# Kernel tuning notes

Measured on AMD Instinct MI355X. Metric: run time of the kernel, lower is better.

## Reference

```python
import jax, jax.numpy as jnp
import numpy as np

B, S, D, H, P = 2, 2048, 1024, 16, 2048  # batch, q_len, d_model, heads, past_len
DEPTH = D // H
W_STD = 0.02


def setup_inputs() -> dict:
    key = jax.random.key(0)
    ks = jax.random.split(key, 5)
    x = jax.random.normal(ks[0], (B, S, D), dtype=jnp.float32)
    past_layer = jax.random.normal(ks[1], (B, 2, H, P, DEPTH), dtype=jnp.float32)
    w_attn = jax.random.normal(ks[2], (D, 3 * D), dtype=jnp.float32) * W_STD
    b_attn = jnp.zeros((3 * D,), dtype=jnp.float32)
    w_proj = jax.random.normal(ks[3], (D, D), dtype=jnp.float32) * W_STD
    b_proj = jnp.zeros((D,), dtype=jnp.float32)
    # causal mask with KV cache: query i sits at absolute position P+i; key j
    # is masked (1.0 -> +(-1e9)) when j > P + i.
    q_pos = P + jnp.arange(S)[:, None]        # [S,1]
    k_pos = jnp.arange(P + S)[None, :]        # [1,P+S]
    mask = (k_pos > q_pos).astype(jnp.float32)[None, None]  # [1,1,S,P+S]
    return {"x": x, "mask": mask, "past_layer": past_layer,
            "w_attn": w_attn, "b_attn": b_attn,
            "w_proj": w_proj, "b_proj": b_proj}


def _split_heads(t):
    # [B,S,D] -> [B,H,S,depth]
    b, s, _ = t.shape
    return t.reshape(b, s, H, DEPTH).transpose(0, 2, 1, 3)


def reference(x, mask, past_layer, w_attn, b_attn, w_proj, b_proj):
    # fused QKV projection (Conv1d == pointwise Linear)
    qkv = jnp.einsum('bsd,de->bse', x, w_attn) + b_attn        # [B,S,3D]
    q, k, v = jnp.split(qkv, 3, axis=2)
    q, k, v = _split_heads(q), _split_heads(k), _split_heads(v)
    # KV-cache concat
    k = jnp.concatenate([past_layer[:, 0], k], axis=2)         # [B,H,P+S,depth]
    v = jnp.concatenate([past_layer[:, 1], v], axis=2)
    present = jnp.stack([k, v], axis=1)                        # [B,2,H,P+S,depth]
    # scaled dot-product attention (full score matrix, eval mode: no dropout)
    scores = jnp.einsum('bhqd,bhkd->bhqk', q, k) / jnp.sqrt(
        jnp.asarray(DEPTH, dtype=jnp.float32))
    scores = scores + mask * (-1e9)
    attn = jax.nn.softmax(scores, axis=-1)
    ctx = jnp.einsum('bhqk,bhkd->bhqd', attn, v)               # [B,H,S,depth]
    merged = ctx.transpose(0, 2, 1, 3).reshape(B, S, D)
    output = jnp.einsum('bsd,de->bse', merged, w_proj) + b_proj
    return output, present
```

## Files before the change

kernel.cpp:

```cpp
#include <hip/hip_runtime.h>
#include <hip/hip_bf16.h>

#define B_ 2
#define S_ 2048
#define D_ 1024
#define H_ 16
#define P_ 2048
#define T_ 4096
#define DEPTH_ 64

typedef __bf16 bf16x8 __attribute__((ext_vector_type(8)));
typedef float  f32x4  __attribute__((ext_vector_type(4)));
typedef short  short8_t __attribute__((ext_vector_type(8)));
typedef unsigned short ushort_t;
typedef unsigned short ushort4_t __attribute__((ext_vector_type(4)));

__device__ __forceinline__ ushort_t f2bf(float f) {
    union { float f; unsigned u; } v; v.f = f;
    return (ushort_t)((v.u + 0x7fffu + ((v.u >> 16) & 1u)) >> 16);
}

__device__ __forceinline__ unsigned cvt_pk_bf16(float lo, float hi) {
    unsigned r;
    asm("v_cvt_pk_bf16_f32 %0, %1, %2" : "=v"(r) : "v"(lo), "v"(hi));
    return r;
}

__device__ __forceinline__ void gload16(const void* g, void* l) {
    __builtin_amdgcn_global_load_lds(
        (const __attribute__((address_space(1))) unsigned int*)g,
        (__attribute__((address_space(3))) unsigned int*)l, 16, 0, 0);
}

__global__ __launch_bounds__(256)
void convert_bf16_kernel(const float4* __restrict__ in, ushort4_t* __restrict__ out, int n4)
{
    for (int i = blockIdx.x * 256 + threadIdx.x; i < n4; i += gridDim.x * 256) {
        float4 v = in[i];
        ushort4_t o;
        o[0] = f2bf(v.x); o[1] = f2bf(v.y); o[2] = f2bf(v.z); o[3] = f2bf(v.w);
        out[i] = o;
    }
}

__global__ __launch_bounds__(256)
void transpose_conv_kernel(const float* __restrict__ w, ushort_t* __restrict__ wt, int N)
{
    __shared__ float t[64][65];
    const int tid = threadIdx.x;
    const int k0 = blockIdx.y * 64, n0 = blockIdx.x * 64;
    #pragma unroll
    for (int rep = 0; rep < 4; ++rep) {
        const int idx = rep * 256 + tid;
        const int r = idx >> 4, c = idx & 15;
        float4 v = *(const float4*)&w[(size_t)(k0 + r) * N + n0 + c * 4];
        t[r][c*4+0] = v.x; t[r][c*4+1] = v.y; t[r][c*4+2] = v.z; t[r][c*4+3] = v.w;
    }
    __syncthreads();
    #pragma unroll
    for (int rep = 0; rep < 4; ++rep) {
        const int idx = rep * 256 + tid;
        const int nl = idx >> 4, kg = idx & 15;
        ushort4_t o;
        o[0] = f2bf(t[kg*4+0][nl]); o[1] = f2bf(t[kg*4+1][nl]);
        o[2] = f2bf(t[kg*4+2][nl]); o[3] = f2bf(t[kg*4+3][nl]);
        *(ushort4_t*)&wt[(size_t)(n0 + nl) * 1024 + k0 + kg*4] = o;
    }
}

template<int MODE>
__global__ __launch_bounds__(256)
void gemm_bf16_kernel(const ushort_t* __restrict__ A,
                      const ushort_t* __restrict__ Bt,
                      const float*  __restrict__ bias,
                      ushort_t* __restrict__ out_qb,
                      float*  __restrict__ out_present,
                      float*  __restrict__ out_plain)
{
    __shared__ __attribute__((aligned(16))) ushort_t As[128*32];
    __shared__ __attribute__((aligned(16))) ushort_t Bs[128*32];

    const int tid  = threadIdx.x;
    const int w    = tid >> 6;
    const int lane = tid & 63;
    const int g    = lane >> 4;
    const int ln   = lane & 15;
    const int wr   = w >> 1, wc = w & 1;
    const int row0 = blockIdx.y * 128;
    const int col0 = blockIdx.x * 128;

    int srow[2], sgl[2];
    #pragma unroll
    for (int r = 0; r < 2; ++r) {
        const int o = (w*2 + r) * 1024 + lane * 16;
        srow[r] = o >> 6;
        const int gp = (o >> 4) & 3;
        sgl[r] = gp ^ ((srow[r] >> 1) & 3);
    }

    f32x4 acc[4][4];
    #pragma unroll
    for (int i = 0; i < 4; ++i)
        #pragma unroll
        for (int j = 0; j < 4; ++j)
            acc[i][j] = (f32x4){0.f, 0.f, 0.f, 0.f};

    for (int k0 = 0; k0 < 1024; k0 += 32) {
        #pragma unroll
        for (int r = 0; r < 2; ++r) {
            const int lb = (w*2 + r) * 512;
            gload16(&A [(size_t)(row0 + srow[r]) * 1024 + k0 + sgl[r]*8], &As[lb]);
            gload16(&Bt[(size_t)(col0 + srow[r]) * 1024 + k0 + sgl[r]*8], &Bs[lb]);
        }
        __syncthreads();

        bf16x8 af[4], bfr[4];
        #pragma unroll
        for (int i = 0; i < 4; ++i) {
            const int ra = wr*64 + i*16 + ln;
            const int ga = g ^ ((ra >> 1) & 3);
            af[i] = __builtin_bit_cast(bf16x8, *(const short8_t*)&As[ra*32 + ga*8]);
            const int rb = wc*64 + i*16 + ln;
            const int gb = g ^ ((rb >> 1) & 3);
            bfr[i] = __builtin_bit_cast(bf16x8, *(const short8_t*)&Bs[rb*32 + gb*8]);
        }
        #pragma unroll
        for (int i = 0; i < 4; ++i)
            #pragma unroll
            for (int j = 0; j < 4; ++j)
                acc[i][j] = __builtin_amdgcn_mfma_f32_16x16x32_bf16(af[i], bfr[j], acc[i][j], 0, 0, 0);
        __syncthreads();
    }

    #pragma unroll
    for (int i = 0; i < 4; ++i) {
        #pragma unroll
        for (int j = 0; j < 4; ++j) {
            const int rm = row0 + wr*64 + i*16 + g*4 + j;
            const int b  = rm >> 11;
            const int s  = rm & 2047;
            #pragma unroll
            for (int jn = 0; jn < 4; ++jn) {
                const int e = col0 + wc*64 + jn*16 + ln;
                const float v = acc[i][jn][j] + bias[e];
                if (MODE == 0) {
                    const int which = e >> 10;
                    const int f = e & 1023;
                    const int h = f >> 6, d = f & 63;
                    if (which == 0) {
                        out_qb[(size_t)(((b*16 + h) * 2048 + s) << 6) + d] =
                            f2bf(v * 0.18033688f);
                    } else {
                        const int kv = which - 1;
                        out_present[((((size_t)(b*2 + kv)*16 + h) * 4096 + 2048 + s) << 6) + d] = v;
                    }
                } else {
                    out_plain[(size_t)rm * 1024 + e] = v;
                }
            }
        }
    }
}

__global__ __launch_bounds__(256)
void prep_kv_kernel(const float* __restrict__ past,
                    float* __restrict__ present,
                    ushort_t* __restrict__ Kws, ushort_t* __restrict__ Vws)
{
    __shared__ float tv[64][65];
    const int tid = threadIdx.x;
    const int kt  = blockIdx.x;
    const int bh  = blockIdx.y;
    const int b   = bh >> 4, h = bh & 15;
    const bool old = (kt < 32);

    const float* Kp = old ? past    + (((size_t)(b*2+0)*16 + h) * P_ + kt*64) * 64
                          : present + (((size_t)(b*2+0)*16 + h) * T_ + kt*64) * 64;
    const float* Vp = old ? past    + (((size_t)(b*2+1)*16 + h) * P_ + kt*64) * 64
                          : present + (((size_t)(b*2+1)*16 + h) * T_ + kt*64) * 64;
    float4* PKo = (float4*)(present + (((size_t)(b*2+0)*16 + h) * T_ + kt*64) * 64);
    float4* PVo = (float4*)(present + (((size_t)(b*2+1)*16 + h) * T_ + kt*64) * 64);
    ushort_t* Kd = Kws + ((size_t)bh * T_ + kt*64) * 64;

    #pragma unroll
    for (int rep = 0; rep < 4; ++rep) {
        const int idx = rep * 256 + tid;
        float4 v = ((const float4*)Kp)[idx];
        if (old) PKo[idx] = v;
        ushort4_t o;
        o[0] = f2bf(v.x); o[1] = f2bf(v.y); o[2] = f2bf(v.z); o[3] = f2bf(v.w);
        *(ushort4_t*)&Kd[idx*4] = o;
        float4 vv = ((const float4*)Vp)[idx];
        if (old) PVo[idx] = vv;
        const int r = idx >> 4, c = idx & 15;
        tv[r][c*4+0] = vv.x; tv[r][c*4+1] = vv.y;
        tv[r][c*4+2] = vv.z; tv[r][c*4+3] = vv.w;
    }
    __syncthreads();
    #pragma unroll
    for (int rep = 0; rep < 4; ++rep) {
        const int idx = rep * 256 + tid;
        const int d = idx >> 4, pg = idx & 15;
        ushort4_t o;
        o[0] = f2bf(tv[pg*4+0][d]); o[1] = f2bf(tv[pg*4+1][d]);
        o[2] = f2bf(tv[pg*4+2][d]); o[3] = f2bf(tv[pg*4+3][d]);
        *(ushort4_t*)&Vws[((size_t)bh*64 + d) * T_ + kt*64 + pg*4] = o;
    }
}

__global__ __launch_bounds__(256, 4)
void attn_v9_kernel(const ushort_t* __restrict__ qin,
                    const ushort_t* __restrict__ Kws,
                    const ushort_t* __restrict__ Vws,
                    ushort_t* __restrict__ merged)
{
    __shared__ __attribute__((aligned(16))) ushort_t Kb0[4096];
    __shared__ __attribute__((aligned(16))) ushort_t Kb1[4096];
    __shared__ __attribute__((aligned(16))) ushort_t Vb0[4096];
    __shared__ __attribute__((aligned(16))) ushort_t Vb1[4096];

    const int tid  = threadIdx.x;
    const int w    = tid >> 6;
    const int lane = tid & 63;
    const int g    = lane >> 4;
    const int ln   = lane & 15;
    const int lnm  = ln & 7;
    const int lsub = lane >> 3;
    const int swz8 = ((lane & 7) ^ lsub) * 8;

    const int bid = (int)blockIdx.x;
    const int a   = bid & 7;
    const int m_c = (bid >> 3) & 31;
    const int j   = bid >> 8;
    const int bh  = a * 4 + (m_c & 3);
    const int c   = m_c >> 2;
    const int qblk = (j == 0) ? c : (j == 1) ? (15 - c) : (j == 2) ? (16 + c) : (31 - c);
    const int q0   = qblk * 64;
    const int b    = bh >> 4, h = bh & 15;

    const ushort_t* Kbase = Kws + (size_t)bh * T_ * 64;
    const ushort_t* Vbase = Vws + (size_t)bh * 64 * T_;
    const int nt = 33 + qblk;

    const int kgOff0 = ((w*16 + 0 + lsub) << 6) + swz8;
    const int kgOff1 = ((w*16 + 8 + lsub) << 6) + swz8;
    const size_t vgOff0 = (size_t)(w*16 + 0 + lsub) * T_ + swz8;
    const size_t vgOff1 = (size_t)(w*16 + 8 + lsub) * T_ + swz8;
    const int ldsOff0 = (w*2 + 0) * 512;
    const int ldsOff1 = (w*2 + 1) * 512;
    const int pRow = (w*16 + ln) * 64;

    gload16(Kbase + kgOff0, &Kb0[ldsOff0]);
    gload16(Kbase + kgOff1, &Kb0[ldsOff1]);
    gload16(Vbase + vgOff0, &Vb0[ldsOff0]);
    gload16(Vbase + vgOff1, &Vb0[ldsOff1]);

    bf16x8 qf[2];
    {
        const ushort_t* Qr = qin + ((size_t)bh * S_ + q0 + w*16 + ln) * 64;
        #pragma unroll
        for (int kh = 0; kh < 2; ++kh)
            qf[kh] = __builtin_bit_cast(bf16x8, *(const short8_t*)(Qr + kh*32 + g*8));
    }

    f32x4 o[4];
    #pragma unroll
    for (int d = 0; d < 4; ++d) o[d] = (f32x4){0.f, 0.f, 0.f, 0.f};
    float m = -3.0e38f, l = 0.f;

#define ATTN_BODY(KBUF, VBUF, NBUF_K, NBUF_V)                                   \
    {                                                                           \
                    \
        asm volatile("s_waitcnt vmcnt(2)" ::: "memory");                        \
        __builtin_amdgcn_s_barrier();                                           \
        __builtin_amdgcn_sched_barrier(0);                                      \
        const bool haspf = (t + 1 < nt);                                        \
        if (haspf) {                                                            \
            const size_t t0n = (size_t)(t + 1) * 64;                            \
            gload16(Kbase + (t0n << 6) + kgOff0, &NBUF_K[ldsOff0]);             \
            gload16(Kbase + (t0n << 6) + kgOff1, &NBUF_K[ldsOff1]);             \
            gload16(Vbase + vgOff0 + t0n, &NBUF_V[ldsOff0]);                    \
            gload16(Vbase + vgOff1 + t0n, &NBUF_V[ldsOff1]);                    \
            __builtin_amdgcn_sched_barrier(0);                                  \
        }                                                                       \
        f32x4 st[4];                                                            \
        __builtin_amdgcn_s_setprio(1);                                          \
        _Pragma("unroll")                                                       \
        for (int js = 0; js < 4; ++js) {                                        \
            const ushort_t* kr = &KBUF[(js*16 + ln) * 64];                      \
            bf16x8 a0 = __builtin_bit_cast(bf16x8, *(const short8_t*)(kr + ((    g) ^ lnm)*8)); \
            bf16x8 a1 = __builtin_bit_cast(bf16x8, *(const short8_t*)(kr + ((4 + g) ^ lnm)*8)); \
            f32x4 z = (f32x4){0.f, 0.f, 0.f, 0.f};                              \
            z = __builtin_amdgcn_mfma_f32_16x16x32_bf16(a0, qf[0], z, 0, 0, 0); \
            z = __builtin_amdgcn_mfma_f32_16x16x32_bf16(a1, qf[1], z, 0, 0, 0); \
            st[js] = z;                                                         \
        }                                                                       \
        __builtin_amdgcn_s_setprio(0);                                          \
        if (t == nt - 1) {                                                      \
            const int qr = w*16 + ln;                                           \
            _Pragma("unroll")                                                   \
            for (int js = 0; js < 4; ++js)                                      \
                _Pragma("unroll")                                               \
                for (int r = 0; r < 4; ++r)                                     \
                    if (js*16 + g*4 + r > qr) st[js][r] = -1e30f;               \
        }                                                                       \
                  \
        float mj[4];                                                            \
        _Pragma("unroll")                                                       \
        for (int js = 0; js < 4; ++js) {                                        \
            float m01 = fmaxf(st[js][0], st[js][1]);                            \
            mj[js] = fmaxf(fmaxf(m01, st[js][2]), st[js][3]);                   \
        }                                                                       \
        float mx16 = fmaxf(fmaxf(fmaxf(mj[0], mj[1]), mj[2]), mj[3]);           \
        if (!__all(mx16 <= m + 8.0f)) {                                         \
            float gmx = fmaxf(mx16, __shfl_xor(mx16, 16));                      \
            gmx = fmaxf(gmx, __shfl_xor(gmx, 32));                              \
            const float mnew = fmaxf(m, gmx);                                   \
            const float corr = exp2f(m - mnew);                                 \
            m = mnew;                                                           \
            l *= corr;                                                          \
            _Pragma("unroll")                                                   \
            for (int d = 0; d < 4; ++d)                                         \
                _Pragma("unroll")                                               \
                for (int r = 0; r < 4; ++r)                                     \
                    o[d][r] *= corr;                                            \
        }                                                                       \
            \
        if (haspf) { asm volatile("s_waitcnt vmcnt(4)" ::: "memory"); }         \
        else       { asm volatile("s_waitcnt vmcnt(0)" ::: "memory"); }         \
        __builtin_amdgcn_s_barrier();                                           \
        __builtin_amdgcn_sched_barrier(0);                                      \
        float rs = 0.f;                                                         \
        _Pragma("unroll")                                                       \
        for (int js = 0; js < 4; ++js) {                                        \
            float p0 = exp2f(st[js][0] - m);                                    \
            float p1 = exp2f(st[js][1] - m);                                    \
            float p2 = exp2f(st[js][2] - m);                                    \
            float p3 = exp2f(st[js][3] - m);                                    \
            rs += (p0 + p1) + (p2 + p3);                                        \
            uint2 pk;                                                           \
            pk.x = cvt_pk_bf16(p0, p1);                                         \
            pk.y = cvt_pk_bf16(p2, p3);                                         \
            *(uint2*)&KBUF[pRow + (((js*4 + g) ^ (lnm << 1)) << 2)] = pk;       \
        }                                                                       \
        l += rs;                                                                \
        __builtin_amdgcn_s_setprio(1);                                          \
        _Pragma("unroll")                                                       \
        for (int kh = 0; kh < 2; ++kh) {                                        \
            bf16x8 pfr = __builtin_bit_cast(bf16x8,                             \
                           *(const short8_t*)&KBUF[pRow + (((kh*4 + g) ^ lnm) << 3)]); \
            _Pragma("unroll")                                                   \
            for (int dsub = 0; dsub < 4; ++dsub) {                              \
                const ushort_t* vr = &VBUF[(dsub*16 + ln) * 64];                \
                bf16x8 va = __builtin_bit_cast(bf16x8,                          \
                              *(const short8_t*)(vr + ((kh*4 + g) ^ lnm)*8));   \
                o[dsub] = __builtin_amdgcn_mfma_f32_16x16x32_bf16(va, pfr, o[dsub], 0, 0, 0); \
            }                                                                   \
        }                                                                       \
        __builtin_amdgcn_s_setprio(0);                                          \
    }

    int t = 0;
    for (;;) {
        ATTN_BODY(Kb0, Vb0, Kb1, Vb1);
        if (++t == nt) break;
        ATTN_BODY(Kb1, Vb1, Kb0, Vb0);
        if (++t == nt) break;
    }
#undef ATTN_BODY

    float lf = l + __shfl_xor(l, 16);
    lf = lf + __shfl_xor(lf, 32);
    const float inv = 1.f / lf;
    const int row = q0 + w*16 + ln;
    #pragma unroll
    for (int dsub = 0; dsub < 4; ++dsub) {
        ushort4_t ov;
        ov[0] = f2bf(o[dsub][0] * inv);
        ov[1] = f2bf(o[dsub][1] * inv);
        ov[2] = f2bf(o[dsub][2] * inv);
        ov[3] = f2bf(o[dsub][3] * inv);
        *(ushort4_t*)&merged[((size_t)b * S_ + row) * D_ + h*64 + dsub*16 + g*4] = ov;
    }
}

extern "C" void kernel_launch(void* const* d_in, const int* in_sizes, int n_in,
                              void* d_out, int out_size, void* d_ws, size_t ws_size,
                              hipStream_t stream)
{
    const float* x      = (const float*)d_in[0];
    const float* past   = (const float*)d_in[2];
    const float* w_attn = (const float*)d_in[3];
    const float* b_attn = (const float*)d_in[4];
    const float* w_proj = (const float*)d_in[5];
    const float* b_proj = (const float*)d_in[6];

    float* out     = (float*)d_out;
    float* present = out + (size_t)B_ * S_ * D_;

    ushort_t* wsu     = (ushort_t*)d_ws;
    ushort_t* q_ws    = wsu;
    ushort_t* mergedb = wsu + 4194304;
    ushort_t* wptb    = wsu + 8388608;
    ushort_t* xb      = wsu + 9437184;
    ushort_t* watb    = wsu + 13631488;
    ushort_t* K_ws    = wsu + 9437184;
    ushort_t* V_ws    = wsu + 17825792;

    convert_bf16_kernel<<<2048, 256, 0, stream>>>(
        (const float4*)x, (ushort4_t*)xb, (B_*S_*D_)/4);
    transpose_conv_kernel<<<dim3(48, 16), 256, 0, stream>>>(w_attn, watb, 3072);
    transpose_conv_kernel<<<dim3(16, 16), 256, 0, stream>>>(w_proj, wptb, 1024);

    gemm_bf16_kernel<0><<<dim3(24, 32), 256, 0, stream>>>(
        xb, watb, b_attn, q_ws, present, nullptr);

    prep_kv_kernel<<<dim3(64, 32), 256, 0, stream>>>(past, present, K_ws, V_ws);

    attn_v9_kernel<<<dim3(1024), 256, 0, stream>>>(q_ws, K_ws, V_ws, mergedb);

    gemm_bf16_kernel<1><<<dim3(8, 32), 256, 0, stream>>>(
        mergedb, wptb, b_proj, nullptr, nullptr, out);
}
```

Measured before the change: 200.9 us.

## Process 128 query rows per attention block to reuse K/V tiles

The attention kernel now handles 128 query rows per block instead of 64, with each wave owning two 16-row query groups that share the K and V fragments loaded from LDS. The grid is halved to 512 blocks and launch bounds drop to 2 blocks per CU. The P matrix moves to a dedicated LDS buffer, which lets the softmax exponentials be written before the barrier rather than after it. This cuts K/V global and LDS traffic per query, at the cost of more registers, more LDS, fewer resident waves, and a shared running max across the two row groups, which may cause extra rescaling.

```diff
diff --git a/kernel.cpp b/kernel.cpp
--- a/kernel.cpp
+++ b/kernel.cpp
@@ -208,16 +208,17 @@
     }
 }
 
-__global__ __launch_bounds__(256, 4)
-void attn_v9_kernel(const ushort_t* __restrict__ qin,
-                    const ushort_t* __restrict__ Kws,
-                    const ushort_t* __restrict__ Vws,
-                    ushort_t* __restrict__ merged)
+__global__ __launch_bounds__(256, 2)
+void attn_v10_kernel(const ushort_t* __restrict__ qin,
+                     const ushort_t* __restrict__ Kws,
+                     const ushort_t* __restrict__ Vws,
+                     ushort_t* __restrict__ merged)
 {
     __shared__ __attribute__((aligned(16))) ushort_t Kb0[4096];
     __shared__ __attribute__((aligned(16))) ushort_t Kb1[4096];
     __shared__ __attribute__((aligned(16))) ushort_t Vb0[4096];
     __shared__ __attribute__((aligned(16))) ushort_t Vb1[4096];
+    __shared__ __attribute__((aligned(16))) ushort_t Pb[128*64];
 
     const int tid  = threadIdx.x;
     const int w    = tid >> 6;
@@ -234,13 +235,13 @@
     const int j   = bid >> 8;
     const int bh  = a * 4 + (m_c & 3);
     const int c   = m_c >> 2;
-    const int qblk = (j == 0) ? c : (j == 1) ? (15 - c) : (j == 2) ? (16 + c) : (31 - c);
-    const int q0   = qblk * 64;
+    const int qblk = (j == 0) ? c : (15 - c);
+    const int q0   = qblk * 128;
     const int b    = bh >> 4, h = bh & 15;
 
     const ushort_t* Kbase = Kws + (size_t)bh * T_ * 64;
     const ushort_t* Vbase = Vws + (size_t)bh * 64 * T_;
-    const int nt = 33 + qblk;
+    const int nt = 34 + 2 * qblk;
 
     const int kgOff0 = ((w*16 + 0 + lsub) << 6) + swz8;
     const int kgOff1 = ((w*16 + 8 + lsub) << 6) + swz8;
@@ -248,29 +249,33 @@
     const size_t vgOff1 = (size_t)(w*16 + 8 + lsub) * T_ + swz8;
     const int ldsOff0 = (w*2 + 0) * 512;
     const int ldsOff1 = (w*2 + 1) * 512;
-    const int pRow = (w*16 + ln) * 64;
+    const int pRow0 = (w*32 + ln) * 64;
+    const int pRow1 = (w*32 + 16 + ln) * 64;
 
     gload16(Kbase + kgOff0, &Kb0[ldsOff0]);
     gload16(Kbase + kgOff1, &Kb0[ldsOff1]);
     gload16(Vbase + vgOff0, &Vb0[ldsOff0]);
     gload16(Vbase + vgOff1, &Vb0[ldsOff1]);
 
-    bf16x8 qf[2];
-    {
-        const ushort_t* Qr = qin + ((size_t)bh * S_ + q0 + w*16 + ln) * 64;
+    bf16x8 qf[2][2];
+    #pragma unroll
+    for (int qg = 0; qg < 2; ++qg) {
+        const ushort_t* Qr = qin + ((size_t)bh * S_ + q0 + w*32 + qg*16 + ln) * 64;
         #pragma unroll
         for (int kh = 0; kh < 2; ++kh)
-            qf[kh] = __builtin_bit_cast(bf16x8, *(const short8_t*)(Qr + kh*32 + g*8));
-    }
-
-    f32x4 o[4];
-    #pragma unroll
-    for (int d = 0; d < 4; ++d) o[d] = (f32x4){0.f, 0.f, 0.f, 0.f};
-    float m = -3.0e38f, l = 0.f;
+            qf[qg][kh] = __builtin_bit_cast(bf16x8, *(const short8_t*)(Qr + kh*32 + g*8));
+    }
+
+    f32x4 o[2][4];
+    #pragma unroll
+    for (int qg = 0; qg < 2; ++qg)
+        #pragma unroll
+        for (int d = 0; d < 4; ++d) o[qg][d] = (f32x4){0.f, 0.f, 0.f, 0.f};
+    float m = -3.0e38f;
+    float l0 = 0.f, l1 = 0.f;
 
 #define ATTN_BODY(KBUF, VBUF, NBUF_K, NBUF_V)                                   \
     {                                                                           \
-                    \
         asm volatile("s_waitcnt vmcnt(2)" ::: "memory");                        \
         __builtin_amdgcn_s_barrier();                                           \
         __builtin_amdgcn_sched_barrier(0);                                      \
@@ -283,78 +288,95 @@
             gload16(Vbase + vgOff1 + t0n, &NBUF_V[ldsOff1]);                    \
             __builtin_amdgcn_sched_barrier(0);                                  \
         }                                                                       \
-        f32x4 st[4];                                                            \
+        f32x4 st[2][4];                                                         \
         __builtin_amdgcn_s_setprio(1);                                          \
         _Pragma("unroll")                                                       \
         for (int js = 0; js < 4; ++js) {                                        \
             const ushort_t* kr = &KBUF[(js*16 + ln) * 64];                      \
             bf16x8 a0 = __builtin_bit_cast(bf16x8, *(const short8_t*)(kr + ((    g) ^ lnm)*8)); \
             bf16x8 a1 = __builtin_bit_cast(bf16x8, *(const short8_t*)(kr + ((4 + g) ^ lnm)*8)); \
-            f32x4 z = (f32x4){0.f, 0.f, 0.f, 0.f};                              \
-            z = __builtin_amdgcn_mfma_f32_16x16x32_bf16(a0, qf[0], z, 0, 0, 0); \
-            z = __builtin_amdgcn_mfma_f32_16x16x32_bf16(a1, qf[1], z, 0, 0, 0); \
-            st[js] = z;                                                         \
+            _Pragma("unroll")                                                   \
+            for (int qg = 0; qg < 2; ++qg) {                                    \
+                f32x4 z = (f32x4){0.f, 0.f, 0.f, 0.f};                          \
+                z = __builtin_amdgcn_mfma_f32_16x16x32_bf16(a0, qf[qg][0], z, 0, 0, 0); \
+                z = __builtin_amdgcn_mfma_f32_16x16x32_bf16(a1, qf[qg][1], z, 0, 0, 0); \
+                st[qg][js] = z;                                                 \
+            }                                                                   \
         }                                                                       \
         __builtin_amdgcn_s_setprio(0);                                          \
-        if (t == nt - 1) {                                                      \
-            const int qr = w*16 + ln;                                           \
-            _Pragma("unroll")                                                   \
-            for (int js = 0; js < 4; ++js)                                      \
+        if (t >= nt - 2) {                                                      \
+            const int off = t*64 - 2048 - q0;                                   \
+            _Pragma("unroll")                                                   \
+            for (int qg = 0; qg < 2; ++qg) {                                    \
+                const int wrow = w*32 + qg*16 + ln;                             \
                 _Pragma("unroll")                                               \
-                for (int r = 0; r < 4; ++r)                                     \
-                    if (js*16 + g*4 + r > qr) st[js][r] = -1e30f;               \
-        }                                                                       \
-                  \
-        float mj[4];                                                            \
+                for (int js = 0; js < 4; ++js)                                  \
+                    _Pragma("unroll")                                           \
+                    for (int r = 0; r < 4; ++r)                                 \
+                        if (js*16 + g*4 + r + off > wrow) st[qg][js][r] = -1e30f; \
+            }                                                                   \
+        }                                                                       \
+        float mx16 = st[0][0][0];                                               \
         _Pragma("unroll")                                                       \
-        for (int js = 0; js < 4; ++js) {                                        \
-            float m01 = fmaxf(st[js][0], st[js][1]);                            \
-            mj[js] = fmaxf(fmaxf(m01, st[js][2]), st[js][3]);                   \
-        }                                                                       \
-        float mx16 = fmaxf(fmaxf(fmaxf(mj[0], mj[1]), mj[2]), mj[3]);           \
+        for (int qg = 0; qg < 2; ++qg)                                          \
+            _Pragma("unroll")                                                   \
+            for (int js = 0; js < 4; ++js) {                                    \
+                float m01 = fmaxf(st[qg][js][0], st[qg][js][1]);                \
+                float m23 = fmaxf(st[qg][js][2], st[qg][js][3]);                \
+                mx16 = fmaxf(mx16, fmaxf(m01, m23));                            \
+            }                                                                   \
         if (!__all(mx16 <= m + 8.0f)) {                                         \
             float gmx = fmaxf(mx16, __shfl_xor(mx16, 16));                      \
             gmx = fmaxf(gmx, __shfl_xor(gmx, 32));                              \
             const float mnew = fmaxf(m, gmx);                                   \
             const float corr = exp2f(m - mnew);                                 \
             m = mnew;                                                           \
-            l *= corr;                                                          \
-            _Pragma("unroll")                                                   \
-            for (int d = 0; d < 4; ++d)                                         \
+            l0 *= corr; l1 *= corr;                                             \
+            _Pragma("unroll")                                                   \
+            for (int qg = 0; qg < 2; ++qg)                                      \
                 _Pragma("unroll")                                               \
-                for (int r = 0; r < 4; ++r)                                     \
-                    o[d][r] *= corr;                                            \
-        }                                                                       \
-            \
+                for (int d = 0; d < 4; ++d)                                     \
+                    _Pragma("unroll")                                           \
+                    for (int r = 0; r < 4; ++r)                                 \
+                        o[qg][d][r] *= corr;                                    \
+        }                                                                       \
+        _Pragma("unroll")                                                       \
+        for (int qg = 0; qg < 2; ++qg) {                                        \
+            const int pR = qg ? pRow1 : pRow0;                                  \
+            float rs = 0.f;                                                     \
+            _Pragma("unroll")                                                   \
+            for (int js = 0; js < 4; ++js) {                                    \
+                float p0 = exp2f(st[qg][js][0] - m);                            \
+                float p1 = exp2f(st[qg][js][1] - m);                            \
+                float p2 = exp2f(st[qg][js][2] - m);                            \
+                float p3 = exp2f(st[qg][js][3] - m);                            \
+                rs += (p0 + p1) + (p2 + p3);                                    \
+                uint2 pk;                                                       \
+                pk.x = cvt_pk_bf16(p0, p1);                                     \
+                pk.y = cvt_pk_bf16(p2, p3);                                     \
+                *(uint2*)&Pb[pR + (((js*4 + g) ^ (lnm << 1)) << 2)] = pk;       \
+            }                                                                   \
+            if (qg) l1 += rs; else l0 += rs;                                    \
+        }                                                                       \
+                                \
         if (haspf) { asm volatile("s_waitcnt vmcnt(4)" ::: "memory"); }         \
         else       { asm volatile("s_waitcnt vmcnt(0)" ::: "memory"); }         \
         __builtin_amdgcn_s_barrier();                                           \
         __builtin_amdgcn_sched_barrier(0);                                      \
-        float rs = 0.f;                                                         \
-        _Pragma("unroll")                                                       \
-        for (int js = 0; js < 4; ++js) {                                        \
-            float p0 = exp2f(st[js][0] - m);                                    \
-            float p1 = exp2f(st[js][1] - m);                                    \
-            float p2 = exp2f(st[js][2] - m);                                    \
-            float p3 = exp2f(st[js][3] - m);                                    \
-            rs += (p0 + p1) + (p2 + p3);                                        \
-            uint2 pk;                                                           \
-            pk.x = cvt_pk_bf16(p0, p1);                                         \
-            pk.y = cvt_pk_bf16(p2, p3);                                         \
-            *(uint2*)&KBUF[pRow + (((js*4 + g) ^ (lnm << 1)) << 2)] = pk;       \
-        }                                                                       \
-        l += rs;                                                                \
         __builtin_amdgcn_s_setprio(1);                                          \
         _Pragma("unroll")                                                       \
         for (int kh = 0; kh < 2; ++kh) {                                        \
-            bf16x8 pfr = __builtin_bit_cast(bf16x8,                             \
-                           *(const short8_t*)&KBUF[pRow + (((kh*4 + g) ^ lnm) << 3)]); \
+            bf16x8 pf0 = __builtin_bit_cast(bf16x8,                             \
+                           *(const short8_t*)&Pb[pRow0 + (((kh*4 + g) ^ lnm) << 3)]); \
+            bf16x8 pf1 = __builtin_bit_cast(bf16x8,                             \
+                           *(const short8_t*)&Pb[pRow1 + (((kh*4 + g) ^ lnm) << 3)]); \
             _Pragma("unroll")                                                   \
             for (int dsub = 0; dsub < 4; ++dsub) {                              \
                 const ushort_t* vr = &VBUF[(dsub*16 + ln) * 64];                \
                 bf16x8 va = __builtin_bit_cast(bf16x8,                          \
                               *(const short8_t*)(vr + ((kh*4 + g) ^ lnm)*8));   \
-                o[dsub] = __builtin_amdgcn_mfma_f32_16x16x32_bf16(va, pfr, o[dsub], 0, 0, 0); \
+                o[0][dsub] = __builtin_amdgcn_mfma_f32_16x16x32_bf16(va, pf0, o[0][dsub], 0, 0, 0); \
+                o[1][dsub] = __builtin_amdgcn_mfma_f32_16x16x32_bf16(va, pf1, o[1][dsub], 0, 0, 0); \
             }                                                                   \
         }                                                                       \
         __builtin_amdgcn_s_setprio(0);                                          \
@@ -369,18 +391,21 @@
     }
 #undef ATTN_BODY
 
-    float lf = l + __shfl_xor(l, 16);
-    lf = lf + __shfl_xor(lf, 32);
-    const float inv = 1.f / lf;
-    const int row = q0 + w*16 + ln;
-    #pragma unroll
-    for (int dsub = 0; dsub < 4; ++dsub) {
-        ushort4_t ov;
-        ov[0] = f2bf(o[dsub][0] * inv);
-        ov[1] = f2bf(o[dsub][1] * inv);
-        ov[2] = f2bf(o[dsub][2] * inv);
-        ov[3] = f2bf(o[dsub][3] * inv);
-        *(ushort4_t*)&merged[((size_t)b * S_ + row) * D_ + h*64 + dsub*16 + g*4] = ov;
+    float lf0 = l0 + __shfl_xor(l0, 16); lf0 += __shfl_xor(lf0, 32);
+    float lf1 = l1 + __shfl_xor(l1, 16); lf1 += __shfl_xor(lf1, 32);
+    #pragma unroll
+    for (int qg = 0; qg < 2; ++qg) {
+        const float inv = 1.f / (qg ? lf1 : lf0);
+        const int row = q0 + w*32 + qg*16 + ln;
+        #pragma unroll
+        for (int dsub = 0; dsub < 4; ++dsub) {
+            ushort4_t ov;
+            ov[0] = f2bf(o[qg][dsub][0] * inv);
+            ov[1] = f2bf(o[qg][dsub][1] * inv);
+            ov[2] = f2bf(o[qg][dsub][2] * inv);
+            ov[3] = f2bf(o[qg][dsub][3] * inv);
+            *(ushort4_t*)&merged[((size_t)b * S_ + row) * D_ + h*64 + dsub*16 + g*4] = ov;
+        }
     }
 }
 
@@ -417,7 +442,7 @@
 
     prep_kv_kernel<<<dim3(64, 32), 256, 0, stream>>>(past, present, K_ws, V_ws);
 
-    attn_v9_kernel<<<dim3(1024), 256, 0, stream>>>(q_ws, K_ws, V_ws, mergedb);
+    attn_v10_kernel<<<dim3(512), 256, 0, stream>>>(q_ws, K_ws, V_ws, mergedb);
 
     gemm_bf16_kernel<1><<<dim3(8, 32), 256, 0, stream>>>(
         mergedb, wptb, b_proj, nullptr, nullptr, out);
```

Measured after the change: 207.5 us. 3.3% more time.
